# Kernel optimization log

Measured on AMD Instinct MI355X. Metric: run time of the kernel, lower is better.

## Reference

```python
import jax, jax.numpy as jnp
import numpy as np

B, N, HID, E, H = 4, 256, 256, 64, 4
OUT = HID // 2          # 128
D = OUT // H            # 32
AGG = H * (2 * D + 1)   # 260 = concat(mean D, attn_sum 1, max D) per head


def setup_inputs() -> dict:
    key = jax.random.key(0)
    ks = jax.random.split(key, 7)
    s = 0.05
    return {
        "h_x": jax.random.normal(ks[0], (B, N, HID), jnp.float32),
        "h_e": jax.random.normal(ks[1], (B, N, N, E), jnp.float32),
        "h_m": jnp.ones((B, N), jnp.float32),
        "W_Q": jax.random.normal(ks[2], (OUT, HID), jnp.float32) * s,
        "W_K": jax.random.normal(ks[3], (OUT, E), jnp.float32) * s,
        "W_V": jax.random.normal(ks[4], (OUT, E), jnp.float32) * s,
        "W_R": jax.random.normal(ks[5], (OUT, AGG), jnp.float32) * s,
    }


def reference(h_x, h_e, h_m, W_Q, W_K, W_V, W_R):
    # queries from node features: [B,H,N,D]
    h_q = (h_x @ W_Q.T).reshape(B, N, H, D).transpose(0, 2, 1, 3)
    # keys/values from dense pairwise edge features: [B,H,N,N,D]
    h_k = jnp.einsum('bnme,ce->bnmc', h_e, W_K).reshape(B, N, N, H, D).transpose(0, 3, 1, 2, 4)
    h_v = jnp.einsum('bnme,ce->bnmc', h_e, W_V).reshape(B, N, N, H, D).transpose(0, 3, 1, 2, 4)
    # broadcast dot: [B,H,N,N]
    scores = jnp.einsum('bhnd,bhnmd->bhnm', h_q, h_k) / np.float32(np.sqrt(D))
    # per-node mask broadcast as [B,1,N,1] (masks query rows)
    scores = jnp.where(h_m[:, None, :, None] == 0, -jnp.inf, scores)
    # NOTE: original code softmaxes over dim=1 = HEAD axis (faithful)
    attn = jax.nn.softmax(scores, axis=1)                      # [B,H,N,N]
    attn_w = attn[..., None] * h_v                             # [B,H,N,N,D]
    aggr_sum = attn_w.sum(axis=3)                              # [B,H,N,D]
    attn_sum = attn.sum(axis=3, keepdims=True) + 1e-8          # [B,H,N,1]
    aggr_mean = aggr_sum / attn_sum
    aggr_max = attn_w.max(axis=3)                              # [B,H,N,D]
    multi = jnp.concatenate([aggr_mean, attn_sum, aggr_max], axis=-1)  # [B,H,N,2D+1]
    aggr_out = multi.transpose(0, 2, 1, 3).reshape(B, N, AGG)  # [B,N,260]
    return aggr_out @ W_R.T                                    # [B,N,OUT]
```

## Files before the change

kernel.cpp:

```cpp
#include <hip/hip_runtime.h>

constexpr int Bb   = 4;
constexpr int Nn   = 256;
constexpr int HID  = 256;
constexpr int Ee   = 64;
constexpr int Hh   = 4;
constexpr int OUTc = 128;
constexpr int Dd   = 32;
constexpr int AGG  = 260;

constexpr int MT    = 32;
constexpr int TPB   = 2;
constexpr int NTP   = Nn / (MT * TPB);
constexpr int A_LD  = 72;
constexpr int K_LD  = 132;
constexpr int REC   = 264;
constexpr int QA_LD = 264;

constexpr size_t WS_PART  = 0;
constexpr size_t WS_QBUF  = (size_t)Bb * Nn * NTP * REC;
constexpr size_t WS_WRT   = WS_QBUF + (size_t)Bb * Nn * OUTc;
constexpr size_t WS_FRAG  = WS_WRT + (size_t)AGG * OUTc;

typedef __attribute__((ext_vector_type(8))) short short8;
typedef __attribute__((ext_vector_type(4))) float floatx4;

__device__ __forceinline__ unsigned short f2bf(float f) {
    union { float f; unsigned u; } x; x.f = f;
    unsigned r = x.u + 0x7FFFu + ((x.u >> 16) & 1u);
    return (unsigned short)(r >> 16);
}

__device__ __forceinline__ short8 pack8(floatx4 f0, floatx4 f1) {
    short8 v;
    v[0] = (short)f2bf(f0[0]); v[1] = (short)f2bf(f0[1]);
    v[2] = (short)f2bf(f0[2]); v[3] = (short)f2bf(f0[3]);
    v[4] = (short)f2bf(f1[0]); v[5] = (short)f2bf(f1[1]);
    v[6] = (short)f2bf(f1[2]); v[7] = (short)f2bf(f1[3]);
    return v;
}

__global__ __launch_bounds__(256)
void eama_pre(const float* __restrict__ h_x, const float* __restrict__ W_Q,
              const float* __restrict__ W_K, const float* __restrict__ W_V,
              const float* __restrict__ W_R,
              unsigned short* __restrict__ wfragKV, float* __restrict__ W_RT,
              float* __restrict__ qbuf)
{
    __shared__ __align__(16) unsigned short sA[16 * QA_LD];
    const int tid = threadIdx.x;
    const int bid = blockIdx.x;

    if (bid < 8) {
        const int e    = bid * 256 + tid;
        const int lane = e & 63;
        const int ks   = (e >> 6) & 1;
        const int ct   = (e >> 7) & 3;
        const int wv   = (e >> 9) & 3;
        const int ncol = lane & 15, q8 = lane >> 4;
        const int c = wv * 64 + ct * 16 + ncol;
        const float* row = (c < OUTc) ? (W_K + c * Ee) : (W_V + (c - OUTc) * Ee);
        const int k0 = ks * 32 + q8 * 8;
        floatx4 f0 = *(const floatx4*)(row + k0);
        floatx4 f1 = *(const floatx4*)(row + k0 + 4);
        *(short8*)(wfragKV + (size_t)e * 8) = pack8(f0, f1);
    } else if (bid < 138) {
        const int i = (bid - 8) * 256 + tid;
        if (i < AGG * OUTc) {
            const int c = i & 127, j = i >> 7;
            W_RT[j * OUTc + c] = W_R[c * AGG + j];
        }
    } else {
        const int b0   = (bid - 138) * 16;
        const int lane = tid & 63;
        const int wv   = tid >> 6;
        const int ncol = lane & 15, q8 = lane >> 4;

        short8 bq[2][8];
        #pragma unroll
        for (int ct = 0; ct < 2; ++ct) {
            const int c = wv * 32 + ct * 16 + ncol;
            const float* row = W_Q + c * HID;
            #pragma unroll
            for (int ks = 0; ks < 8; ++ks) {
                const int k0 = ks * 32 + q8 * 8;
                floatx4 f0 = *(const floatx4*)(row + k0);
                floatx4 f1 = *(const floatx4*)(row + k0 + 4);
                bq[ct][ks] = pack8(f0, f1);
            }
        }
        #pragma unroll
        for (int i = 0; i < 2; ++i) {
            const int idx = tid + i * 256;
            const int r = idx >> 5, blk = idx & 31;
            const float* src = h_x + (size_t)(b0 + r) * HID + blk * 8;
            floatx4 f0 = *(const floatx4*)(src);
            floatx4 f1 = *(const floatx4*)(src + 4);
            *(short8*)&sA[r * QA_LD + blk * 8] = pack8(f0, f1);
        }
        __syncthreads();
        floatx4 acc[2] = {(floatx4){0,0,0,0}, (floatx4){0,0,0,0}};
        #pragma unroll
        for (int ks = 0; ks < 8; ++ks) {
            short8 a = *(const short8*)&sA[ncol * QA_LD + ks * 32 + q8 * 8];
            acc[0] = __builtin_amdgcn_mfma_f32_16x16x32_bf16(a, bq[0][ks], acc[0], 0, 0, 0);
            acc[1] = __builtin_amdgcn_mfma_f32_16x16x32_bf16(a, bq[1][ks], acc[1], 0, 0, 0);
        }
        #pragma unroll
        for (int ct = 0; ct < 2; ++ct)
            #pragma unroll
            for (int rr = 0; rr < 4; ++rr)
                qbuf[(size_t)(b0 + q8 * 4 + rr) * OUTc + wv * 32 + ct * 16 + ncol] = acc[ct][rr];
    }
}

__global__ __launch_bounds__(256, 4)
void eama_stage1(const float* __restrict__ h_e, const float* __restrict__ h_m,
                 const unsigned short* __restrict__ wfragKV,
                 const float* __restrict__ qbuf, float* __restrict__ wsP)
{
    __shared__ __align__(16) unsigned short sA[MT * A_LD];
    __shared__ __align__(16) float sK[MT * K_LD];
    __shared__ __align__(16) float sQ[OUTc];
    __shared__ float sSc[MT][4];
    __shared__ float sAt[MT][4];

    const int tid  = threadIdx.x;
    const int lane = tid & 63;
    const int wv   = tid >> 6;
    const int ncol = lane & 15;
    const int q8   = lane >> 4;
    const int bn   = blockIdx.x;
    const int tp   = blockIdx.y;
    const float maskv = h_m[bn];

    if (tid < OUTc) sQ[tid] = qbuf[bn * OUTc + tid];

    const float* heb = h_e + ((size_t)bn * Nn + tp * (MT * TPB)) * Ee;
    const int r = tid >> 3, blk = tid & 7;
    floatx4 pf[TPB][2];
    #pragma unroll
    for (int it = 0; it < TPB; ++it) {
        const float* src = heb + (it * MT + r) * Ee + blk * 8;
        pf[it][0] = *(const floatx4*)(src);
        pf[it][1] = *(const floatx4*)(src + 4);
    }

    short8 bfrag[4][2];
    #pragma unroll
    for (int ct = 0; ct < 4; ++ct)
        #pragma unroll
        for (int ks = 0; ks < 2; ++ks) {
            const int e = ((wv * 4 + ct) * 2 + ks) * 64 + lane;
            bfrag[ct][ks] = *(const short8*)(wfragKV + (size_t)e * 8);
        }

    float vs[4], vm[4], asum = 0.f;
    #pragma unroll
    for (int ct = 0; ct < 4; ++ct) { vs[ct] = 0.f; vm[ct] = -3.402823466e38f; }

    for (int it = 0; it < TPB; ++it) {
        *(short8*)&sA[r * A_LD + blk * 8] = pack8(pf[it][0], pf[it][1]);
        __syncthreads();

        floatx4 acc[2][4];
        #pragma unroll
        for (int mt = 0; mt < 2; ++mt)
            #pragma unroll
            for (int ct = 0; ct < 4; ++ct)
                acc[mt][ct] = (floatx4){0.f, 0.f, 0.f, 0.f};
        #pragma unroll
        for (int ks = 0; ks < 2; ++ks) {
            short8 a0 = *(const short8*)&sA[(ncol) * A_LD + ks * 32 + q8 * 8];
            short8 a1 = *(const short8*)&sA[(16 + ncol) * A_LD + ks * 32 + q8 * 8];
            #pragma unroll
            for (int ct = 0; ct < 4; ++ct) {
                acc[0][ct] = __builtin_amdgcn_mfma_f32_16x16x32_bf16(a0, bfrag[ct][ks], acc[0][ct], 0, 0, 0);
                acc[1][ct] = __builtin_amdgcn_mfma_f32_16x16x32_bf16(a1, bfrag[ct][ks], acc[1][ct], 0, 0, 0);
            }
        }
        if (wv < 2) {
            #pragma unroll
            for (int mt = 0; mt < 2; ++mt) {
                const int rowb = mt * 16 + q8 * 4;
                #pragma unroll
                for (int ct = 0; ct < 4; ++ct) {
                    const int col = wv * 64 + ct * 16 + ncol;
                    #pragma unroll
                    for (int rr = 0; rr < 4; ++rr)
                        sK[(rowb + rr) * K_LD + col] = acc[mt][ct][rr];
                }
            }
        }
        __syncthreads();

        if (tid < 128) {
            const int m = tid & 31, h = tid >> 5;
            const float* kr = &sK[m * K_LD + h * Dd];
            const float* qr = &sQ[h * Dd];
            float p = 0.f;
            #pragma unroll
            for (int d = 0; d < Dd; d += 4) {
                floatx4 k4 = *(const floatx4*)(kr + d);
                floatx4 q4 = *(const floatx4*)(qr + d);
                p += k4[0]*q4[0] + k4[1]*q4[1] + k4[2]*q4[2] + k4[3]*q4[3];
            }
            p *= 0.1767766952966369f;
            sSc[m][h] = (maskv != 0.f) ? p : -1e30f;
        }
        __syncthreads();

        if (tid < MT) {
            float s0 = sSc[tid][0], s1 = sSc[tid][1], s2 = sSc[tid][2], s3 = sSc[tid][3];
            float mx = fmaxf(fmaxf(s0, s1), fmaxf(s2, s3));
            float e0 = __expf(s0 - mx), e1 = __expf(s1 - mx);
            float e2 = __expf(s2 - mx), e3 = __expf(s3 - mx);
            float inv = 1.f / (e0 + e1 + e2 + e3);
            sAt[tid][0] = e0 * inv; sAt[tid][1] = e1 * inv;
            sAt[tid][2] = e2 * inv; sAt[tid][3] = e3 * inv;
        }
        __syncthreads();

        if (wv >= 2) {
            #pragma unroll
            for (int ct = 0; ct < 4; ++ct) {
                const int hd = (wv - 2) * 2 + (ct >> 1);
                #pragma unroll
                for (int mt = 0; mt < 2; ++mt) {
                    const int rowb = mt * 16 + q8 * 4;
                    #pragma unroll
                    for (int rr = 0; rr < 4; ++rr) {
                        const float aw = sAt[rowb + rr][hd] * acc[mt][ct][rr];
                        vs[ct] += aw;
                        vm[ct] = fmaxf(vm[ct], aw);
                    }
                }
            }
        }
        if (tid < Hh) {
            #pragma unroll
            for (int m = 0; m < MT; ++m) asum += sAt[m][tid];
        }
    }

    const size_t base = ((size_t)bn * NTP + tp) * REC;
    if (wv >= 2) {
        #pragma unroll
        for (int ct = 0; ct < 4; ++ct) {
            vs[ct] += __shfl_xor(vs[ct], 16, 64);
            vs[ct] += __shfl_xor(vs[ct], 32, 64);
            vm[ct] = fmaxf(vm[ct], __shfl_xor(vm[ct], 16, 64));
            vm[ct] = fmaxf(vm[ct], __shfl_xor(vm[ct], 32, 64));
        }
        if (lane < 16) {
            #pragma unroll
            for (int ct = 0; ct < 4; ++ct) {
                const int cv = (wv - 2) * 64 + ct * 16 + ncol;
                wsP[base + cv]        = vs[ct];
                wsP[base + OUTc + cv] = vm[ct];
            }
        }
    }
    if (tid < Hh) wsP[base + 2 * OUTc + tid] = asum;
}

__global__ __launch_bounds__(128)
void eama_stage2(const float* __restrict__ wsP, const float* __restrict__ W_RT,
                 float* __restrict__ out)
{
    __shared__ __align__(16) float sM[REC];
    __shared__ float sAs[Hh];
    const int tid = threadIdx.x;
    const int bn  = blockIdx.x;
    const size_t base = (size_t)bn * NTP * REC;

    float vsum = 0.f, vmax = -3.402823466e38f;
    #pragma unroll
    for (int tp = 0; tp < NTP; ++tp) {
        vsum += wsP[base + tp * REC + tid];
        vmax = fmaxf(vmax, wsP[base + tp * REC + OUTc + tid]);
    }
    if (tid < Hh) {
        float a = 1e-8f;
        #pragma unroll
        for (int tp = 0; tp < NTP; ++tp) a += wsP[base + tp * REC + 2 * OUTc + tid];
        sAs[tid] = a;
    }
    __syncthreads();
    {
        const int h = tid >> 5, d = tid & 31;
        sM[h * 65 + d]      = vsum / sAs[h];
        sM[h * 65 + 33 + d] = vmax;
        if (tid < Hh) sM[tid * 65 + 32] = sAs[tid];
    }
    __syncthreads();
    {
        float acc = 0.f;
        #pragma unroll 4
        for (int j = 0; j < AGG; ++j)
            acc = fmaf(sM[j], W_RT[j * OUTc + tid], acc);
        out[bn * OUTc + tid] = acc;
    }
}

extern "C" void kernel_launch(void* const* d_in, const int* in_sizes, int n_in,
                              void* d_out, int out_size, void* d_ws, size_t ws_size,
                              hipStream_t stream) {
    const float* h_x = (const float*)d_in[0];
    const float* h_e = (const float*)d_in[1];
    const float* h_m = (const float*)d_in[2];
    const float* W_Q = (const float*)d_in[3];
    const float* W_K = (const float*)d_in[4];
    const float* W_V = (const float*)d_in[5];
    const float* W_R = (const float*)d_in[6];
    float* out = (float*)d_out;

    float* ws            = (float*)d_ws;
    float* wsP           = ws + WS_PART;
    float* qbuf          = ws + WS_QBUF;
    float* W_RT          = ws + WS_WRT;
    unsigned short* wfKV = (unsigned short*)(ws + WS_FRAG);

    eama_pre<<<dim3(138 + Bb * Nn / 16), dim3(256), 0, stream>>>(
        h_x, W_Q, W_K, W_V, W_R, wfKV, W_RT, qbuf);
    eama_stage1<<<dim3(Bb * Nn, NTP), dim3(256), 0, stream>>>(h_e, h_m, wfKV, qbuf, wsP);
    eama_stage2<<<dim3(Bb * Nn), dim3(128), 0, stream>>>(wsP, W_RT, out);
}
```

Before: 139.8 us.

## Fold W_K into per-node query vector and restructure stage1 around register softmax

Precomputes u = W_K^T q per node and head in a new kernel, so scores come from h_e·u directly and the full K projection is never formed. Stage1 is rewritten so each wave loads its own h_e rows straight into MFMA fragments, computes V and scores together, and does the head-axis softmax with lane shuffles instead of shared-memory round trips and barriers. The grid is halved to two m-halves per node, with a cross-wave reduction through shared memory, and stage2's dot product is split into four accumulators. It adds one extra kernel launch and raises register pressure in stage1, where the occupancy hint drops from 4 to 2.

Result: faster. 129.9 us (-7.1%).

```diff
diff --git a/kernel.cpp b/kernel.cpp
--- a/kernel.cpp
+++ b/kernel.cpp
@@ -8,19 +8,14 @@
 constexpr int OUTc = 128;
 constexpr int Dd   = 32;
 constexpr int AGG  = 260;
-
-constexpr int MT    = 32;
-constexpr int TPB   = 2;
-constexpr int NTP   = Nn / (MT * TPB);
-constexpr int A_LD  = 72;
-constexpr int K_LD  = 132;
-constexpr int REC   = 264;
+constexpr int REC  = 264;
 constexpr int QA_LD = 264;
 
 constexpr size_t WS_PART  = 0;
-constexpr size_t WS_QBUF  = (size_t)Bb * Nn * NTP * REC;
+constexpr size_t WS_QBUF  = WS_PART + (size_t)Bb * Nn * 2 * REC;
 constexpr size_t WS_WRT   = WS_QBUF + (size_t)Bb * Nn * OUTc;
-constexpr size_t WS_FRAG  = WS_WRT + (size_t)AGG * OUTc;
+constexpr size_t WS_FRAGV = WS_WRT + (size_t)AGG * OUTc;
+constexpr size_t WS_UFRAG = WS_FRAGV + 4096;
 
 typedef __attribute__((ext_vector_type(8))) short short8;
 typedef __attribute__((ext_vector_type(4))) float floatx4;
@@ -42,36 +37,33 @@
 
 __global__ __launch_bounds__(256)
 void eama_pre(const float* __restrict__ h_x, const float* __restrict__ W_Q,
-              const float* __restrict__ W_K, const float* __restrict__ W_V,
-              const float* __restrict__ W_R,
-              unsigned short* __restrict__ wfragKV, float* __restrict__ W_RT,
+              const float* __restrict__ W_V, const float* __restrict__ W_R,
+              unsigned short* __restrict__ wfragV, float* __restrict__ W_RT,
               float* __restrict__ qbuf)
 {
     __shared__ __align__(16) unsigned short sA[16 * QA_LD];
     const int tid = threadIdx.x;
     const int bid = blockIdx.x;
 
-    if (bid < 8) {
+    if (bid < 4) {
         const int e    = bid * 256 + tid;
         const int lane = e & 63;
         const int ks   = (e >> 6) & 1;
-        const int ct   = (e >> 7) & 3;
-        const int wv   = (e >> 9) & 3;
+        const int ct   = e >> 7;
         const int ncol = lane & 15, q8 = lane >> 4;
-        const int c = wv * 64 + ct * 16 + ncol;
-        const float* row = (c < OUTc) ? (W_K + c * Ee) : (W_V + (c - OUTc) * Ee);
+        const float* row = W_V + (ct * 16 + ncol) * Ee;
         const int k0 = ks * 32 + q8 * 8;
         floatx4 f0 = *(const floatx4*)(row + k0);
         floatx4 f1 = *(const floatx4*)(row + k0 + 4);
-        *(short8*)(wfragKV + (size_t)e * 8) = pack8(f0, f1);
-    } else if (bid < 138) {
-        const int i = (bid - 8) * 256 + tid;
+        *(short8*)(wfragV + (size_t)e * 8) = pack8(f0, f1);
+    } else if (bid < 134) {
+        const int i = (bid - 4) * 256 + tid;
         if (i < AGG * OUTc) {
             const int c = i & 127, j = i >> 7;
             W_RT[j * OUTc + c] = W_R[c * AGG + j];
         }
     } else {
-        const int b0   = (bid - 138) * 16;
+        const int b0   = (bid - 134) * 16;
         const int lane = tid & 63;
         const int wv   = tid >> 6;
         const int ncol = lane & 15, q8 = lane >> 4;
@@ -114,154 +106,159 @@
     }
 }
 
-__global__ __launch_bounds__(256, 4)
+__global__ __launch_bounds__(256)
+void eama_u(const float* __restrict__ qbuf, const float* __restrict__ W_K,
+            unsigned short* __restrict__ ufrag)
+{
+    __shared__ float sq[OUTc];
+    __shared__ __align__(16) float sU[Hh][Ee];
+    const int tid = threadIdx.x;
+    const int bn  = blockIdx.x;
+    if (tid < OUTc) sq[tid] = qbuf[bn * OUTc + tid];
+    __syncthreads();
+    {
+        const int h = tid >> 6, e = tid & 63;
+        float a0 = 0.f, a1 = 0.f;
+        #pragma unroll
+        for (int d = 0; d < Dd; d += 2) {
+            a0 = fmaf(sq[h * Dd + d],     W_K[(h * Dd + d) * Ee + e],     a0);
+            a1 = fmaf(sq[h * Dd + d + 1], W_K[(h * Dd + d + 1) * Ee + e], a1);
+        }
+        sU[h][e] = (a0 + a1) * 0.1767766952966369f;
+    }
+    __syncthreads();
+    if (tid < 128) {
+        const int ks = tid >> 6, l = tid & 63;
+        const int nc = l & 15, q8 = l >> 4;
+        short8 v = {0,0,0,0,0,0,0,0};
+        if (nc < Hh) {
+            const float* u = &sU[nc][ks * 32 + q8 * 8];
+            floatx4 f0 = *(const floatx4*)u;
+            floatx4 f1 = *(const floatx4*)(u + 4);
+            v = pack8(f0, f1);
+        }
+        *(short8*)(ufrag + ((size_t)(bn * 2 + ks) * 64 + l) * 8) = v;
+    }
+}
+
+__global__ __launch_bounds__(256, 2)
 void eama_stage1(const float* __restrict__ h_e, const float* __restrict__ h_m,
-                 const unsigned short* __restrict__ wfragKV,
-                 const float* __restrict__ qbuf, float* __restrict__ wsP)
+                 const unsigned short* __restrict__ wfragV,
+                 const unsigned short* __restrict__ ufrag,
+                 float* __restrict__ wsP)
 {
-    __shared__ __align__(16) unsigned short sA[MT * A_LD];
-    __shared__ __align__(16) float sK[MT * K_LD];
-    __shared__ __align__(16) float sQ[OUTc];
-    __shared__ float sSc[MT][4];
-    __shared__ float sAt[MT][4];
+    __shared__ float sVS[4][OUTc];
+    __shared__ float sVM[4][OUTc];
+    __shared__ float sAS[4][Hh];
 
     const int tid  = threadIdx.x;
     const int lane = tid & 63;
-    const int wv   = tid >> 6;
+    const int w    = tid >> 6;
     const int ncol = lane & 15;
     const int q8   = lane >> 4;
     const int bn   = blockIdx.x;
-    const int tp   = blockIdx.y;
+    const int hf   = blockIdx.y;
     const float maskv = h_m[bn];
 
-    if (tid < OUTc) sQ[tid] = qbuf[bn * OUTc + tid];
-
-    const float* heb = h_e + ((size_t)bn * Nn + tp * (MT * TPB)) * Ee;
-    const int r = tid >> 3, blk = tid & 7;
-    floatx4 pf[TPB][2];
+    short8 bfV[8][2];
     #pragma unroll
-    for (int it = 0; it < TPB; ++it) {
-        const float* src = heb + (it * MT + r) * Ee + blk * 8;
-        pf[it][0] = *(const floatx4*)(src);
-        pf[it][1] = *(const floatx4*)(src + 4);
-    }
-
-    short8 bfrag[4][2];
+    for (int ct = 0; ct < 8; ++ct)
+        #pragma unroll
+        for (int ks = 0; ks < 2; ++ks)
+            bfV[ct][ks] = *(const short8*)(wfragV + ((size_t)(ct * 2 + ks) * 64 + lane) * 8);
+    short8 bu[2];
+    bu[0] = *(const short8*)(ufrag + ((size_t)(bn * 2 + 0) * 64 + lane) * 8);
+    bu[1] = *(const short8*)(ufrag + ((size_t)(bn * 2 + 1) * 64 + lane) * 8);
+
+    float vs[8], vm[8], asum = 0.f;
     #pragma unroll
-    for (int ct = 0; ct < 4; ++ct)
+    for (int ct = 0; ct < 8; ++ct) { vs[ct] = 0.f; vm[ct] = -3.402823466e38f; }
+
+    const float* heb = h_e + (size_t)bn * Nn * Ee;
+
+    #pragma unroll
+    for (int it = 0; it < 2; ++it) {
+        const int m0 = hf * 128 + w * 32 + it * 16;
+        const float* ar = heb + (size_t)(m0 + ncol) * Ee;
+        short8 af[2];
         #pragma unroll
         for (int ks = 0; ks < 2; ++ks) {
-            const int e = ((wv * 4 + ct) * 2 + ks) * 64 + lane;
-            bfrag[ct][ks] = *(const short8*)(wfragKV + (size_t)e * 8);
-        }
-
-    float vs[4], vm[4], asum = 0.f;
+            floatx4 f0 = *(const floatx4*)(ar + ks * 32 + q8 * 8);
+            floatx4 f1 = *(const floatx4*)(ar + ks * 32 + q8 * 8 + 4);
+            af[ks] = pack8(f0, f1);
+        }
+        floatx4 accV[8], accS = (floatx4){0,0,0,0};
+        #pragma unroll
+        for (int ct = 0; ct < 8; ++ct) accV[ct] = (floatx4){0,0,0,0};
+        #pragma unroll
+        for (int ks = 0; ks < 2; ++ks) {
+            #pragma unroll
+            for (int ct = 0; ct < 8; ++ct)
+                accV[ct] = __builtin_amdgcn_mfma_f32_16x16x32_bf16(af[ks], bfV[ct][ks], accV[ct], 0, 0, 0);
+            accS = __builtin_amdgcn_mfma_f32_16x16x32_bf16(af[ks], bu[ks], accS, 0, 0, 0);
+        }
+        float a[4];
+        #pragma unroll
+        for (int r = 0; r < 4; ++r) {
+            float s = (maskv != 0.f) ? accS[r] : -1e30f;
+            float m1 = fmaxf(s, __shfl_xor(s, 1, 64));
+            m1 = fmaxf(m1, __shfl_xor(m1, 2, 64));
+            float e = __expf(s - m1);
+            float t = e + __shfl_xor(e, 1, 64);
+            t += __shfl_xor(t, 2, 64);
+            a[r] = e / t;
+        }
+        asum += a[0] + a[1] + a[2] + a[3];
+        #pragma unroll
+        for (int h = 0; h < Hh; ++h) {
+            const int src = (lane & 48) | h;
+            float aw0 = __shfl(a[0], src, 64);
+            float aw1 = __shfl(a[1], src, 64);
+            float aw2 = __shfl(a[2], src, 64);
+            float aw3 = __shfl(a[3], src, 64);
+            #pragma unroll
+            for (int g = 0; g < 2; ++g) {
+                const int ct = h * 2 + g;
+                float p0 = aw0 * accV[ct][0];
+                float p1 = aw1 * accV[ct][1];
+                float p2 = aw2 * accV[ct][2];
+                float p3 = aw3 * accV[ct][3];
+                vs[ct] += (p0 + p1) + (p2 + p3);
+                vm[ct] = fmaxf(vm[ct], fmaxf(fmaxf(p0, p1), fmaxf(p2, p3)));
+            }
+        }
+    }
+
     #pragma unroll
-    for (int ct = 0; ct < 4; ++ct) { vs[ct] = 0.f; vm[ct] = -3.402823466e38f; }
-
-    for (int it = 0; it < TPB; ++it) {
-        *(short8*)&sA[r * A_LD + blk * 8] = pack8(pf[it][0], pf[it][1]);
-        __syncthreads();
-
-        floatx4 acc[2][4];
-        #pragma unroll
-        for (int mt = 0; mt < 2; ++mt)
-            #pragma unroll
-            for (int ct = 0; ct < 4; ++ct)
-                acc[mt][ct] = (floatx4){0.f, 0.f, 0.f, 0.f};
-        #pragma unroll
-        for (int ks = 0; ks < 2; ++ks) {
-            short8 a0 = *(const short8*)&sA[(ncol) * A_LD + ks * 32 + q8 * 8];
-            short8 a1 = *(const short8*)&sA[(16 + ncol) * A_LD + ks * 32 + q8 * 8];
-            #pragma unroll
-            for (int ct = 0; ct < 4; ++ct) {
-                acc[0][ct] = __builtin_amdgcn_mfma_f32_16x16x32_bf16(a0, bfrag[ct][ks], acc[0][ct], 0, 0, 0);
-                acc[1][ct] = __builtin_amdgcn_mfma_f32_16x16x32_bf16(a1, bfrag[ct][ks], acc[1][ct], 0, 0, 0);
-            }
-        }
-        if (wv < 2) {
-            #pragma unroll
-            for (int mt = 0; mt < 2; ++mt) {
-                const int rowb = mt * 16 + q8 * 4;
-                #pragma unroll
-                for (int ct = 0; ct < 4; ++ct) {
-                    const int col = wv * 64 + ct * 16 + ncol;
-                    #pragma unroll
-                    for (int rr = 0; rr < 4; ++rr)
-                        sK[(rowb + rr) * K_LD + col] = acc[mt][ct][rr];
-                }
-            }
-        }
-        __syncthreads();
-
-        if (tid < 128) {
-            const int m = tid & 31, h = tid >> 5;
-            const float* kr = &sK[m * K_LD + h * Dd];
-            const float* qr = &sQ[h * Dd];
-            float p = 0.f;
-            #pragma unroll
-            for (int d = 0; d < Dd; d += 4) {
-                floatx4 k4 = *(const floatx4*)(kr + d);
-                floatx4 q4 = *(const floatx4*)(qr + d);
-                p += k4[0]*q4[0] + k4[1]*q4[1] + k4[2]*q4[2] + k4[3]*q4[3];
-            }
-            p *= 0.1767766952966369f;
-            sSc[m][h] = (maskv != 0.f) ? p : -1e30f;
-        }
-        __syncthreads();
-
-        if (tid < MT) {
-            float s0 = sSc[tid][0], s1 = sSc[tid][1], s2 = sSc[tid][2], s3 = sSc[tid][3];
-            float mx = fmaxf(fmaxf(s0, s1), fmaxf(s2, s3));
-            float e0 = __expf(s0 - mx), e1 = __expf(s1 - mx);
-            float e2 = __expf(s2 - mx), e3 = __expf(s3 - mx);
-            float inv = 1.f / (e0 + e1 + e2 + e3);
-            sAt[tid][0] = e0 * inv; sAt[tid][1] = e1 * inv;
-            sAt[tid][2] = e2 * inv; sAt[tid][3] = e3 * inv;
-        }
-        __syncthreads();
-
-        if (wv >= 2) {
-            #pragma unroll
-            for (int ct = 0; ct < 4; ++ct) {
-                const int hd = (wv - 2) * 2 + (ct >> 1);
-                #pragma unroll
-                for (int mt = 0; mt < 2; ++mt) {
-                    const int rowb = mt * 16 + q8 * 4;
-                    #pragma unroll
-                    for (int rr = 0; rr < 4; ++rr) {
-                        const float aw = sAt[rowb + rr][hd] * acc[mt][ct][rr];
-                        vs[ct] += aw;
-                        vm[ct] = fmaxf(vm[ct], aw);
-                    }
-                }
-            }
-        }
-        if (tid < Hh) {
-            #pragma unroll
-            for (int m = 0; m < MT; ++m) asum += sAt[m][tid];
-        }
-    }
-
-    const size_t base = ((size_t)bn * NTP + tp) * REC;
-    if (wv >= 2) {
-        #pragma unroll
-        for (int ct = 0; ct < 4; ++ct) {
-            vs[ct] += __shfl_xor(vs[ct], 16, 64);
-            vs[ct] += __shfl_xor(vs[ct], 32, 64);
-            vm[ct] = fmaxf(vm[ct], __shfl_xor(vm[ct], 16, 64));
-            vm[ct] = fmaxf(vm[ct], __shfl_xor(vm[ct], 32, 64));
-        }
-        if (lane < 16) {
-            #pragma unroll
-            for (int ct = 0; ct < 4; ++ct) {
-                const int cv = (wv - 2) * 64 + ct * 16 + ncol;
-                wsP[base + cv]        = vs[ct];
-                wsP[base + OUTc + cv] = vm[ct];
-            }
-        }
-    }
-    if (tid < Hh) wsP[base + 2 * OUTc + tid] = asum;
+    for (int ct = 0; ct < 8; ++ct) {
+        vs[ct] += __shfl_xor(vs[ct], 16, 64);
+        vs[ct] += __shfl_xor(vs[ct], 32, 64);
+        vm[ct] = fmaxf(vm[ct], __shfl_xor(vm[ct], 16, 64));
+        vm[ct] = fmaxf(vm[ct], __shfl_xor(vm[ct], 32, 64));
+    }
+    asum += __shfl_xor(asum, 16, 64);
+    asum += __shfl_xor(asum, 32, 64);
+
+    if (lane < 16) {
+        #pragma unroll
+        for (int ct = 0; ct < 8; ++ct) {
+            sVS[w][ct * 16 + lane] = vs[ct];
+            sVM[w][ct * 16 + lane] = vm[ct];
+        }
+    }
+    if (lane < Hh) sAS[w][lane] = asum;
+    __syncthreads();
+    if (tid < OUTc) {
+        const size_t base = (size_t)(bn * 2 + hf) * REC;
+        float vsum = (sVS[0][tid] + sVS[1][tid]) + (sVS[2][tid] + sVS[3][tid]);
+        float vmax = fmaxf(fmaxf(sVS[0][tid], sVS[0][tid]), 0.f);
+        vmax = fmaxf(fmaxf(sVM[0][tid], sVM[1][tid]), fmaxf(sVM[2][tid], sVM[3][tid]));
+        wsP[base + tid]        = vsum;
+        wsP[base + OUTc + tid] = vmax;
+        if (tid < Hh)
+            wsP[base + 2 * OUTc + tid] =
+                (sAS[0][tid] + sAS[1][tid]) + (sAS[2][tid] + sAS[3][tid]);
+    }
 }
 
 __global__ __launch_bounds__(128)
@@ -272,20 +269,12 @@
     __shared__ float sAs[Hh];
     const int tid = threadIdx.x;
     const int bn  = blockIdx.x;
-    const size_t base = (size_t)bn * NTP * REC;
-
-    float vsum = 0.f, vmax = -3.402823466e38f;
-    #pragma unroll
-    for (int tp = 0; tp < NTP; ++tp) {
-        vsum += wsP[base + tp * REC + tid];
-        vmax = fmaxf(vmax, wsP[base + tp * REC + OUTc + tid]);
-    }
-    if (tid < Hh) {
-        float a = 1e-8f;
-        #pragma unroll
-        for (int tp = 0; tp < NTP; ++tp) a += wsP[base + tp * REC + 2 * OUTc + tid];
-        sAs[tid] = a;
-    }
+    const size_t base = (size_t)bn * 2 * REC;
+
+    float vsum = wsP[base + tid] + wsP[base + REC + tid];
+    float vmax = fmaxf(wsP[base + OUTc + tid], wsP[base + REC + OUTc + tid]);
+    if (tid < Hh)
+        sAs[tid] = wsP[base + 2 * OUTc + tid] + wsP[base + REC + 2 * OUTc + tid] + 1e-8f;
     __syncthreads();
     {
         const int h = tid >> 5, d = tid & 31;
@@ -295,11 +284,15 @@
     }
     __syncthreads();
     {
-        float acc = 0.f;
-        #pragma unroll 4
-        for (int j = 0; j < AGG; ++j)
-            acc = fmaf(sM[j], W_RT[j * OUTc + tid], acc);
-        out[bn * OUTc + tid] = acc;
+        float a0 = 0.f, a1 = 0.f, a2 = 0.f, a3 = 0.f;
+        #pragma unroll 5
+        for (int j = 0; j < AGG; j += 4) {
+            a0 = fmaf(sM[j],     W_RT[(j)     * OUTc + tid], a0);
+            a1 = fmaf(sM[j + 1], W_RT[(j + 1) * OUTc + tid], a1);
+            a2 = fmaf(sM[j + 2], W_RT[(j + 2) * OUTc + tid], a2);
+            a3 = fmaf(sM[j + 3], W_RT[(j + 3) * OUTc + tid], a3);
+        }
+        out[bn * OUTc + tid] = (a0 + a1) + (a2 + a3);
     }
 }
 
@@ -319,10 +312,11 @@
     float* wsP           = ws + WS_PART;
     float* qbuf          = ws + WS_QBUF;
     float* W_RT          = ws + WS_WRT;
-    unsigned short* wfKV = (unsigned short*)(ws + WS_FRAG);
-
-    eama_pre<<<dim3(138 + Bb * Nn / 16), dim3(256), 0, stream>>>(
-        h_x, W_Q, W_K, W_V, W_R, wfKV, W_RT, qbuf);
-    eama_stage1<<<dim3(Bb * Nn, NTP), dim3(256), 0, stream>>>(h_e, h_m, wfKV, qbuf, wsP);
+    unsigned short* wfV  = (unsigned short*)(ws + WS_FRAGV);
+    unsigned short* ufr  = (unsigned short*)(ws + WS_UFRAG);
+
+    eama_pre<<<dim3(198), dim3(256), 0, stream>>>(h_x, W_Q, W_V, W_R, wfV, W_RT, qbuf);
+    eama_u<<<dim3(Bb * Nn), dim3(256), 0, stream>>>(qbuf, W_K, ufr);
+    eama_stage1<<<dim3(Bb * Nn, 2), dim3(256), 0, stream>>>(h_e, h_m, wfV, ufr, wsP);
     eama_stage2<<<dim3(Bb * Nn), dim3(128), 0, stream>>>(wsP, W_RT, out);
 }
```
